# Performance work log

Hardware: AMD Instinct MI355X
Metric: run time of the kernel (lower is better)

Reference implementation:

```python
import jax, jax.numpy as jnp
import numpy as np

B, N, C = 16, 1024, 256
E = 524288
NUM_NODES = B * N
D0 = C + 7            # 263 input node feature dim
LAYERS = [256, 256, 256]


def _xavier(key, shape):
    fan_out, fan_in = shape
    lim = jnp.sqrt(6.0 / (fan_in + fan_out))
    return jax.random.uniform(key, shape, jnp.float32, -lim, lim)


def setup_inputs() -> dict:
    key = jax.random.key(0)
    ks = jax.random.split(key, 9)
    rois = jax.random.normal(ks[0], (B, N, 7), jnp.float32)
    pooled_features = jax.random.normal(ks[1], (B, N, C), jnp.float32)
    edge_index = jax.random.randint(ks[2], (2, E), 0, NUM_NODES, dtype=jnp.int64)
    # EdgeConv linear weights: layer0 in = 2*(C+7)=526, later in = 2*256=512
    W1 = _xavier(ks[3], (LAYERS[0], 2 * D0))
    b1 = jnp.zeros((LAYERS[0],), jnp.float32)
    W2 = _xavier(ks[4], (LAYERS[1], 2 * LAYERS[0]))
    b2 = jnp.zeros((LAYERS[1],), jnp.float32)
    W3 = _xavier(ks[5], (LAYERS[2], 2 * LAYERS[1]))
    b3 = jnp.zeros((LAYERS[2],), jnp.float32)
    return {"rois": rois, "pooled_features": pooled_features,
            "edge_index": edge_index,
            "W1": W1, "b1": b1, "W2": W2, "b2": b2, "W3": W3, "b3": b3}


def _edge_conv(x, src, dst, W, b):
    # message: cat(x_j - x_i, x_i) -> linear -> relu ; aggregate: scatter max at target i
    x_i = x[dst]                                   # [E, d] target features
    x_j = x[src]                                   # [E, d] source features
    msg = jnp.concatenate([x_j - x_i, x_i], axis=-1)   # [E, 2d]
    msg = jax.nn.relu(msg @ W.T + b)               # [E, out]
    agg = jax.ops.segment_max(msg, dst, num_segments=NUM_NODES)
    # nodes with no incoming edges: fill -inf -> 0 (PyG convention)
    return jnp.where(jnp.isfinite(agg), agg, jnp.zeros((), agg.dtype))


def reference(rois, pooled_features, edge_index, W1, b1, W2, b2, W3, b3):
    # global features: cat(pooled, boxes) flattened over batch
    x = jnp.concatenate([pooled_features, rois], axis=-1).reshape(-1, D0)  # [B*N, 263]
    src, dst = edge_index[0], edge_index[1]  # PyG: row = source j, col = target i
    feats = [x]
    x1 = _edge_conv(x, src, dst, W1, b1)
    feats.append(x1)
    x2 = _edge_conv(x1, src, dst, W2, b2)
    feats.append(x2)
    x3 = _edge_conv(x2, src, dst, W3, b3)
    feats.append(x3)
    related_features = jnp.concatenate(feats, axis=-1)  # [B*N, 263+768]
    return related_features
```

## Files before the change

kernel.cpp:

```cpp
#include <hip/hip_runtime.h>
#include <stdint.h>

#define NODES 16384
#define D0    263
#define K1PAD 288
#define OUTW  1031

typedef __attribute__((ext_vector_type(8))) short bf16x8;
typedef __attribute__((ext_vector_type(4))) float f32x4;

__device__ __forceinline__ float bf2f(unsigned short u) {
    union { unsigned int i; float f; } c; c.i = ((unsigned int)u) << 16; return c.f;
}
__device__ __forceinline__ unsigned short f2bf(float f) {
    union { float f; unsigned int i; } c; c.f = f;
    unsigned int x = c.i;
    unsigned int r = (x + 0x7fffu + ((x >> 16) & 1u)) >> 16;
    return (unsigned short)r;
}

__global__ void detect_kernel(const void* __restrict__ ei, const void* __restrict__ pooled,
                              int* __restrict__ flags) {
    int lane = threadIdx.x;
    const long long* e64 = (const long long*)ei;
    bool ok = true;
    for (int i = lane; i < 512; i += 64) {
        long long v = e64[i];
        if (v < 0 || v >= NODES) ok = false;
    }
    unsigned long long b = __ballot(ok);
    const unsigned short* ph = (const unsigned short*)pooled;
    int hits = 0;
    for (int i = lane; i < 512; i += 64) {
        int e = (ph[i] >> 7) & 0xFF;
        if (e >= 0x90) hits++;
    }
    for (int off = 32; off; off >>= 1) hits += __shfl_down(hits, off);
    if (lane == 0) {
        flags[0] = (b == ~0ull) ? 1 : 0;
        flags[1] = (hits > 8) ? 1 : 0;
    }
}

__global__ void hist_kernel(const void* __restrict__ ei, int E, const int* __restrict__ flags,
                            int* __restrict__ deg) {
    int e = blockIdx.x * blockDim.x + threadIdx.x;
    if (e >= E) return;
    int d = flags[0] ? (int)((const long long*)ei)[(size_t)E + e]
                     : ((const int*)ei)[(size_t)E + e];
    atomicAdd(&deg[d], 1);
}

__global__ void scan_kernel(const int* __restrict__ deg, int* __restrict__ offs,
                            int* __restrict__ cursor) {
    __shared__ int part[256];
    int tid = threadIdx.x;
    int base = tid * 64;
    int s = 0;
    for (int i = 0; i < 64; ++i) s += deg[base + i];
    part[tid] = s;
    __syncthreads();
    for (int off = 1; off < 256; off <<= 1) {
        int t = (tid >= off) ? part[tid - off] : 0;
        __syncthreads();
        part[tid] += t;
        __syncthreads();
    }
    int run = (tid > 0) ? part[tid - 1] : 0;
    for (int i = 0; i < 64; ++i) {
        int idx = base + i;
        offs[idx] = run;
        cursor[idx] = run;
        run += deg[idx];
    }
    if (tid == 255) offs[NODES] = run;
}

__global__ void scatter_kernel(const void* __restrict__ ei, int E, const int* __restrict__ flags,
                               int* __restrict__ cursor, int* __restrict__ ssrc) {
    int e = blockIdx.x * blockDim.x + threadIdx.x;
    if (e >= E) return;
    int s, d;
    if (flags[0]) {
        const long long* p = (const long long*)ei;
        s = (int)p[e];
        d = (int)p[(size_t)E + e];
    } else {
        const int* p = (const int*)ei;
        s = p[e];
        d = p[(size_t)E + e];
    }
    int pos = atomicAdd(&cursor[d], 1);
    ssrc[pos] = s;
}

__global__ void build_x0_kernel(const void* __restrict__ pooled, const void* __restrict__ rois,
                                const int* __restrict__ flags,
                                unsigned short* __restrict__ x0p, void* __restrict__ outv) {
    int idx = blockIdx.x * blockDim.x + threadIdx.x;
    int node = idx / K1PAD;
    int k = idx - node * K1PAD;
    if (node >= NODES) return;
    bool f32m = flags[1] != 0;
    float val = 0.f;
    if (k < 256) {
        val = f32m ? ((const float*)pooled)[(size_t)node * 256 + k]
                   : bf2f(((const unsigned short*)pooled)[(size_t)node * 256 + k]);
    } else if (k < D0) {
        val = f32m ? ((const float*)rois)[(size_t)node * 7 + (k - 256)]
                   : bf2f(((const unsigned short*)rois)[(size_t)node * 7 + (k - 256)]);
    }
    x0p[idx] = f2bf(val);
    if (k < D0) {
        if (f32m) ((float*)outv)[(size_t)node * OUTW + k] = val;
        else      ((unsigned short*)outv)[(size_t)node * OUTW + k] = f2bf(val);
    }
}

#define S1 (512 * K1PAD)
#define S2 (512 * 256)
__global__ void prep_all_kernel(const void* __restrict__ W1, const void* __restrict__ W2,
                                const void* __restrict__ W3, const int* __restrict__ flags,
                                unsigned short* __restrict__ wc1,
                                unsigned short* __restrict__ wc2,
                                unsigned short* __restrict__ wc3) {
    int idx = blockIdx.x * blockDim.x + threadIdx.x;
    bool f32m = flags[1] != 0;
    if (idx < S1) {
        int r = idx / K1PAD;
        int k = idx - r * K1PAD;
        unsigned short val = 0;
        if (k < D0) {
            if (r < 256) {
                float a = f32m ? ((const float*)W1)[(size_t)r * 526 + k]
                               : bf2f(((const unsigned short*)W1)[(size_t)r * 526 + k]);
                val = f2bf(a);
            } else {
                size_t ro = (size_t)(r - 256) * 526;
                float a, b;
                if (f32m) { a = ((const float*)W1)[ro + k]; b = ((const float*)W1)[ro + D0 + k]; }
                else      { a = bf2f(((const unsigned short*)W1)[ro + k]);
                            b = bf2f(((const unsigned short*)W1)[ro + D0 + k]); }
                val = f2bf(b - a);
            }
        }
        wc1[idx] = val;
        return;
    }
    idx -= S1;
    const void* W = (idx < S2) ? W2 : W3;
    unsigned short* wc = (idx < S2) ? wc2 : wc3;
    if (idx >= S2) idx -= S2;
    if (idx >= S2) return;
    int r = idx >> 8;
    int k = idx & 255;
    unsigned short val;
    if (r < 256) {
        float a = f32m ? ((const float*)W)[(size_t)r * 512 + k]
                       : bf2f(((const unsigned short*)W)[(size_t)r * 512 + k]);
        val = f2bf(a);
    } else {
        size_t ro = (size_t)(r - 256) * 512;
        float a, b;
        if (f32m) { a = ((const float*)W)[ro + k]; b = ((const float*)W)[ro + 256 + k]; }
        else      { a = bf2f(((const unsigned short*)W)[ro + k]);
                    b = bf2f(((const unsigned short*)W)[ro + 256 + k]); }
        val = f2bf(b - a);
    }
    wc[idx] = val;
}

template <int K>
__global__ __launch_bounds__(256) void gemm_kernel(const unsigned short* __restrict__ A,
                                                   const unsigned short* __restrict__ Wc,
                                                   unsigned short* __restrict__ u_bf,
                                                   float* __restrict__ v_f) {
    int lane = threadIdx.x & 63;
    int wave = threadIdx.x >> 6;
    int row0 = blockIdx.x * 64;
    int col0 = blockIdx.y * 256 + wave * 64;
    int lr = lane & 15;
    int kb = (lane >> 4) * 8;
    const unsigned short* Ap = A + (size_t)(row0 + lr) * K + kb;
    const unsigned short* Wp = Wc + (size_t)(col0 + lr) * K + kb;

    f32x4 acc[4][4];
    #pragma unroll
    for (int i = 0; i < 4; ++i)
        #pragma unroll
        for (int j = 0; j < 4; ++j) acc[i][j] = (f32x4){0.f, 0.f, 0.f, 0.f};

    for (int k0 = 0; k0 < K; k0 += 32) {
        bf16x8 a[4], b[4];
        #pragma unroll
        for (int i = 0; i < 4; ++i) a[i] = *reinterpret_cast<const bf16x8*>(Ap + (size_t)i * 16 * K + k0);
        #pragma unroll
        for (int i = 0; i < 4; ++i) b[i] = *reinterpret_cast<const bf16x8*>(Wp + (size_t)i * 16 * K + k0);
        #pragma unroll
        for (int rb = 0; rb < 4; ++rb)
            #pragma unroll
            for (int cb = 0; cb < 4; ++cb)
                acc[rb][cb] = __builtin_amdgcn_mfma_f32_16x16x32_bf16(a[rb], b[cb], acc[rb][cb], 0, 0, 0);
    }

    bool is_u = (blockIdx.y == 0);
    #pragma unroll
    for (int rb = 0; rb < 4; ++rb) {
        int rbase = row0 + rb * 16 + (lane >> 4) * 4;
        #pragma unroll
        for (int cb = 0; cb < 4; ++cb) {
            int c = col0 + cb * 16 + lr;
            #pragma unroll
            for (int reg = 0; reg < 4; ++reg) {
                float val = acc[rb][cb][reg];
                int r = rbase + reg;
                if (is_u) u_bf[(size_t)r * 256 + c] = f2bf(val);
                else      v_f[(size_t)r * 256 + (c - 256)] = val;
            }
        }
    }
}

__device__ __forceinline__ void maxpack2(float m[8], uint4 p, uint4 q) {
    unsigned pp[4] = {p.x, p.y, p.z, p.w};
    unsigned qq[4] = {q.x, q.y, q.z, q.w};
    #pragma unroll
    for (int w = 0; w < 4; ++w) {
        m[2 * w]     = fmaxf(fmaxf(m[2 * w],     bf2f((unsigned short)(pp[w] & 0xffff))),
                             bf2f((unsigned short)(qq[w] & 0xffff)));
        m[2 * w + 1] = fmaxf(fmaxf(m[2 * w + 1], bf2f((unsigned short)(pp[w] >> 16))),
                             bf2f((unsigned short)(qq[w] >> 16)));
    }
}
__device__ __forceinline__ void maxpack1(float m[8], uint4 p) {
    unsigned pp[4] = {p.x, p.y, p.z, p.w};
    #pragma unroll
    for (int w = 0; w < 4; ++w) {
        m[2 * w]     = fmaxf(m[2 * w],     bf2f((unsigned short)(pp[w] & 0xffff)));
        m[2 * w + 1] = fmaxf(m[2 * w + 1], bf2f((unsigned short)(pp[w] >> 16)));
    }
}

__global__ __launch_bounds__(256) void combine_kernel(const unsigned short* __restrict__ u_bf,
                                                      const float* __restrict__ v_f,
                                                      const void* __restrict__ bias,
                                                      const int* __restrict__ flags,
                                                      const int* __restrict__ offs,
                                                      const int* __restrict__ ssrc,
                                                      unsigned short* __restrict__ x_cur,
                                                      void* __restrict__ outv,
                                                      int col_off) {
    int lane = threadIdx.x & 63;
    int node = blockIdx.x * 4 + (threadIdx.x >> 6);
    int half = lane >> 5;
    int cl = lane & 31;
    int s0 = offs[node];
    int s1 = offs[node + 1];
    bool f32m = flags[1] != 0;

    const uint4* U = (const uint4*)u_bf;
    float m[8];
    #pragma unroll
    for (int j = 0; j < 8; ++j) m[j] = -INFINITY;

    int i = s0 + half;
    for (; i + 6 < s1; i += 8) {
        int sA = ssrc[i], sB = ssrc[i + 2], sC = ssrc[i + 4], sD = ssrc[i + 6];
        uint4 pA = U[(size_t)sA * 32 + cl];
        uint4 pB = U[(size_t)sB * 32 + cl];
        uint4 pC = U[(size_t)sC * 32 + cl];
        uint4 pD = U[(size_t)sD * 32 + cl];
        maxpack2(m, pA, pB);
        maxpack2(m, pC, pD);
    }
    for (; i < s1; i += 2) {
        int s = ssrc[i];
        maxpack1(m, U[(size_t)s * 32 + cl]);
    }

    #pragma unroll
    for (int j = 0; j < 8; ++j) m[j] = fmaxf(m[j], __shfl_xor(m[j], 32));

    int ch0 = cl * 8 + half * 4;
    float mm[4] = {m[half * 4 + 0], m[half * 4 + 1], m[half * 4 + 2], m[half * 4 + 3]};
    float4 v = *(const float4*)(v_f + (size_t)node * 256 + ch0);
    float bb[4];
    if (f32m) {
        const float* bf = (const float*)bias;
        #pragma unroll
        for (int j = 0; j < 4; ++j) bb[j] = bf[ch0 + j];
    } else {
        const unsigned short* bh = (const unsigned short*)bias;
        #pragma unroll
        for (int j = 0; j < 4; ++j) bb[j] = bf2f(bh[ch0 + j]);
    }
    float vv[4] = {v.x, v.y, v.z, v.w};
    float r[4];
    bool nz = (s1 > s0);
    #pragma unroll
    for (int j = 0; j < 4; ++j) r[j] = nz ? fmaxf(mm[j] + vv[j] + bb[j], 0.f) : 0.f;

    unsigned short h[4];
    #pragma unroll
    for (int j = 0; j < 4; ++j) h[j] = f2bf(r[j]);
    uint2 packed;
    packed.x = (unsigned int)h[0] | ((unsigned int)h[1] << 16);
    packed.y = (unsigned int)h[2] | ((unsigned int)h[3] << 16);
    *(uint2*)(x_cur + (size_t)node * 256 + ch0) = packed;

    size_t ob = (size_t)node * OUTW + col_off + ch0;
    if (f32m) {
        float* of = (float*)outv;
        #pragma unroll
        for (int j = 0; j < 4; ++j) of[ob + j] = r[j];
    } else {
        unsigned short* oh = (unsigned short*)outv;
        #pragma unroll
        for (int j = 0; j < 4; ++j) oh[ob + j] = h[j];
    }
}

extern "C" void kernel_launch(void* const* d_in, const int* in_sizes, int n_in,
                              void* d_out, int out_size, void* d_ws, size_t ws_size,
                              hipStream_t stream) {
    const void* rois   = d_in[0];
    const void* pooled = d_in[1];
    const void* ei     = d_in[2];
    const void* W1 = d_in[3];
    const void* b1 = d_in[4];
    const void* W2 = d_in[5];
    const void* b2 = d_in[6];
    const void* W3 = d_in[7];
    const void* b3 = d_in[8];

    const int E = in_sizes[2] / 2;

    char* ws = (char*)d_ws;
    size_t o = 0;
    auto take = [&](size_t bytes) { size_t cur = o; o += (bytes + 255) & ~(size_t)255; return cur; };
    int* flags           = (int*)(ws + take(8));
    int* deg             = (int*)(ws + take(sizeof(int) * NODES));
    int* offs            = (int*)(ws + take(sizeof(int) * (NODES + 1)));
    int* cursor          = (int*)(ws + take(sizeof(int) * NODES));
    int* ssrc            = (int*)(ws + take(sizeof(int) * (size_t)E));
    unsigned short* x0p  = (unsigned short*)(ws + take(2ull * NODES * K1PAD));
    unsigned short* wc1  = (unsigned short*)(ws + take(2ull * 512 * K1PAD));
    unsigned short* wc2  = (unsigned short*)(ws + take(2ull * 512 * 256));
    unsigned short* wc3  = (unsigned short*)(ws + take(2ull * 512 * 256));
    unsigned short* ubf  = (unsigned short*)(ws + take(2ull * NODES * 256));
    float*          vf   = (float*)(ws + take(4ull * NODES * 256));
    unsigned short* xcur = (unsigned short*)(ws + take(2ull * NODES * 256));
    (void)ws_size;

    const int eb = (E + 255) / 256;

    detect_kernel<<<1, 64, 0, stream>>>(ei, pooled, flags);
    hipMemsetAsync(deg, 0, sizeof(int) * NODES, stream);
    hist_kernel<<<eb, 256, 0, stream>>>(ei, E, flags, deg);
    scan_kernel<<<1, 256, 0, stream>>>(deg, offs, cursor);
    scatter_kernel<<<eb, 256, 0, stream>>>(ei, E, flags, cursor, ssrc);

    build_x0_kernel<<<(NODES * K1PAD) / 256, 256, 0, stream>>>(pooled, rois, flags, x0p, d_out);
    prep_all_kernel<<<(S1 + 2 * S2 + 255) / 256, 256, 0, stream>>>(W1, W2, W3, flags, wc1, wc2, wc3);

    gemm_kernel<K1PAD><<<dim3(NODES / 64, 2), 256, 0, stream>>>(x0p, wc1, ubf, vf);
    combine_kernel<<<NODES / 4, 256, 0, stream>>>(ubf, vf, b1, flags, offs, ssrc, xcur, d_out, D0);

    gemm_kernel<256><<<dim3(NODES / 64, 2), 256, 0, stream>>>(xcur, wc2, ubf, vf);
    combine_kernel<<<NODES / 4, 256, 0, stream>>>(ubf, vf, b2, flags, offs, ssrc, xcur, d_out, D0 + 256);

    gemm_kernel<256><<<dim3(NODES / 64, 2), 256, 0, stream>>>(xcur, wc3, ubf, vf);
    combine_kernel<<<NODES / 4, 256, 0, stream>>>(ubf, vf, b3, flags, offs, ssrc, xcur, d_out, D0 + 512);
}
```

Baseline: 258.3 us.

## Store GEMM u-output as order-preserving uint16 keys and fuse setup launches

```diff
diff --git a/kernel.cpp b/kernel.cpp
--- a/kernel.cpp
+++ b/kernel.cpp
@@ -8,6 +8,7 @@
 
 typedef __attribute__((ext_vector_type(8))) short bf16x8;
 typedef __attribute__((ext_vector_type(4))) float f32x4;
+typedef __attribute__((ext_vector_type(8))) unsigned short u16x8;
 
 __device__ __forceinline__ float bf2f(unsigned short u) {
     union { unsigned int i; float f; } c; c.i = ((unsigned int)u) << 16; return c.f;
@@ -18,27 +19,37 @@
     unsigned int r = (x + 0x7fffu + ((x >> 16) & 1u)) >> 16;
     return (unsigned short)r;
 }
-
-__global__ void detect_kernel(const void* __restrict__ ei, const void* __restrict__ pooled,
-                              int* __restrict__ flags) {
-    int lane = threadIdx.x;
-    const long long* e64 = (const long long*)ei;
-    bool ok = true;
-    for (int i = lane; i < 512; i += 64) {
-        long long v = e64[i];
-        if (v < 0 || v >= NODES) ok = false;
-    }
-    unsigned long long b = __ballot(ok);
-    const unsigned short* ph = (const unsigned short*)pooled;
-    int hits = 0;
-    for (int i = lane; i < 512; i += 64) {
-        int e = (ph[i] >> 7) & 0xFF;
-        if (e >= 0x90) hits++;
-    }
-    for (int off = 32; off; off >>= 1) hits += __shfl_down(hits, off);
-    if (lane == 0) {
-        flags[0] = (b == ~0ull) ? 1 : 0;
-        flags[1] = (hits > 8) ? 1 : 0;
+__device__ __forceinline__ unsigned short bf2key(unsigned short b) {
+    return (b & 0x8000u) ? (unsigned short)~b : (unsigned short)(b | 0x8000u);
+}
+__device__ __forceinline__ unsigned short key2bf(unsigned short k) {
+    return (k & 0x8000u) ? (unsigned short)(k ^ 0x8000u) : (unsigned short)~k;
+}
+
+__global__ void detect_zero_kernel(const void* __restrict__ ei, const void* __restrict__ pooled,
+                                   int* __restrict__ flags, int* __restrict__ deg) {
+    int idx = blockIdx.x * 256 + threadIdx.x;
+    deg[idx] = 0;
+    if (blockIdx.x == 0 && threadIdx.x < 64) {
+        int lane = threadIdx.x;
+        const long long* e64 = (const long long*)ei;
+        bool ok = true;
+        for (int i = lane; i < 512; i += 64) {
+            long long v = e64[i];
+            if (v < 0 || v >= NODES) ok = false;
+        }
+        unsigned long long b = __ballot(ok);
+        const unsigned short* ph = (const unsigned short*)pooled;
+        int hits = 0;
+        for (int i = lane; i < 512; i += 64) {
+            int e = (ph[i] >> 7) & 0xFF;
+            if (e >= 0x90) hits++;
+        }
+        for (int off = 32; off; off >>= 1) hits += __shfl_down(hits, off);
+        if (lane == 0) {
+            flags[0] = (b == ~0ull) ? 1 : 0;
+            flags[1] = (hits > 8) ? 1 : 0;
+        }
     }
 }
 
@@ -94,38 +105,36 @@
     ssrc[pos] = s;
 }
 
-__global__ void build_x0_kernel(const void* __restrict__ pooled, const void* __restrict__ rois,
-                                const int* __restrict__ flags,
-                                unsigned short* __restrict__ x0p, void* __restrict__ outv) {
-    int idx = blockIdx.x * blockDim.x + threadIdx.x;
-    int node = idx / K1PAD;
-    int k = idx - node * K1PAD;
-    if (node >= NODES) return;
-    bool f32m = flags[1] != 0;
-    float val = 0.f;
-    if (k < 256) {
-        val = f32m ? ((const float*)pooled)[(size_t)node * 256 + k]
-                   : bf2f(((const unsigned short*)pooled)[(size_t)node * 256 + k]);
-    } else if (k < D0) {
-        val = f32m ? ((const float*)rois)[(size_t)node * 7 + (k - 256)]
-                   : bf2f(((const unsigned short*)rois)[(size_t)node * 7 + (k - 256)]);
-    }
-    x0p[idx] = f2bf(val);
-    if (k < D0) {
-        if (f32m) ((float*)outv)[(size_t)node * OUTW + k] = val;
-        else      ((unsigned short*)outv)[(size_t)node * OUTW + k] = f2bf(val);
-    }
-}
-
+#define T0 (NODES * K1PAD)
 #define S1 (512 * K1PAD)
 #define S2 (512 * 256)
-__global__ void prep_all_kernel(const void* __restrict__ W1, const void* __restrict__ W2,
-                                const void* __restrict__ W3, const int* __restrict__ flags,
-                                unsigned short* __restrict__ wc1,
-                                unsigned short* __restrict__ wc2,
-                                unsigned short* __restrict__ wc3) {
-    int idx = blockIdx.x * blockDim.x + threadIdx.x;
+__global__ void setup_kernel(const void* __restrict__ pooled, const void* __restrict__ rois,
+                             const void* __restrict__ W1, const void* __restrict__ W2,
+                             const void* __restrict__ W3, const int* __restrict__ flags,
+                             unsigned short* __restrict__ x0p, void* __restrict__ outv,
+                             unsigned short* __restrict__ wc1, unsigned short* __restrict__ wc2,
+                             unsigned short* __restrict__ wc3) {
+    int idx = blockIdx.x * 256 + threadIdx.x;
     bool f32m = flags[1] != 0;
+    if (idx < T0) {
+        int node = idx / K1PAD;
+        int k = idx - node * K1PAD;
+        float val = 0.f;
+        if (k < 256) {
+            val = f32m ? ((const float*)pooled)[(size_t)node * 256 + k]
+                       : bf2f(((const unsigned short*)pooled)[(size_t)node * 256 + k]);
+        } else if (k < D0) {
+            val = f32m ? ((const float*)rois)[(size_t)node * 7 + (k - 256)]
+                       : bf2f(((const unsigned short*)rois)[(size_t)node * 7 + (k - 256)]);
+        }
+        x0p[idx] = f2bf(val);
+        if (k < D0) {
+            if (f32m) ((float*)outv)[(size_t)node * OUTW + k] = val;
+            else      ((unsigned short*)outv)[(size_t)node * OUTW + k] = f2bf(val);
+        }
+        return;
+    }
+    idx -= T0;
     if (idx < S1) {
         int r = idx / K1PAD;
         int k = idx - r * K1PAD;
@@ -151,7 +160,6 @@
     const void* W = (idx < S2) ? W2 : W3;
     unsigned short* wc = (idx < S2) ? wc2 : wc3;
     if (idx >= S2) idx -= S2;
-    if (idx >= S2) return;
     int r = idx >> 8;
     int k = idx & 255;
     unsigned short val;
@@ -173,7 +181,7 @@
 template <int K>
 __global__ __launch_bounds__(256) void gemm_kernel(const unsigned short* __restrict__ A,
                                                    const unsigned short* __restrict__ Wc,
-                                                   unsigned short* __restrict__ u_bf,
+                                                   unsigned short* __restrict__ u_key,
                                                    float* __restrict__ v_f) {
     int lane = threadIdx.x & 63;
     int wave = threadIdx.x >> 6;
@@ -214,34 +222,14 @@
             for (int reg = 0; reg < 4; ++reg) {
                 float val = acc[rb][cb][reg];
                 int r = rbase + reg;
-                if (is_u) u_bf[(size_t)r * 256 + c] = f2bf(val);
+                if (is_u) u_key[(size_t)r * 256 + c] = bf2key(f2bf(val));
                 else      v_f[(size_t)r * 256 + (c - 256)] = val;
             }
         }
     }
 }
 
-__device__ __forceinline__ void maxpack2(float m[8], uint4 p, uint4 q) {
-    unsigned pp[4] = {p.x, p.y, p.z, p.w};
-    unsigned qq[4] = {q.x, q.y, q.z, q.w};
-    #pragma unroll
-    for (int w = 0; w < 4; ++w) {
-        m[2 * w]     = fmaxf(fmaxf(m[2 * w],     bf2f((unsigned short)(pp[w] & 0xffff))),
-                             bf2f((unsigned short)(qq[w] & 0xffff)));
-        m[2 * w + 1] = fmaxf(fmaxf(m[2 * w + 1], bf2f((unsigned short)(pp[w] >> 16))),
-                             bf2f((unsigned short)(qq[w] >> 16)));
-    }
-}
-__device__ __forceinline__ void maxpack1(float m[8], uint4 p) {
-    unsigned pp[4] = {p.x, p.y, p.z, p.w};
-    #pragma unroll
-    for (int w = 0; w < 4; ++w) {
-        m[2 * w]     = fmaxf(m[2 * w],     bf2f((unsigned short)(pp[w] & 0xffff)));
-        m[2 * w + 1] = fmaxf(m[2 * w + 1], bf2f((unsigned short)(pp[w] >> 16)));
-    }
-}
-
-__global__ __launch_bounds__(256) void combine_kernel(const unsigned short* __restrict__ u_bf,
+__global__ __launch_bounds__(256) void combine_kernel(const unsigned short* __restrict__ u_key,
                                                       const float* __restrict__ v_f,
                                                       const void* __restrict__ bias,
                                                       const int* __restrict__ flags,
@@ -258,31 +246,37 @@
     int s1 = offs[node + 1];
     bool f32m = flags[1] != 0;
 
-    const uint4* U = (const uint4*)u_bf;
-    float m[8];
-    #pragma unroll
-    for (int j = 0; j < 8; ++j) m[j] = -INFINITY;
+    const u16x8* U = (const u16x8*)u_key;
+    u16x8 mk = (u16x8)0;
 
     int i = s0 + half;
     for (; i + 6 < s1; i += 8) {
         int sA = ssrc[i], sB = ssrc[i + 2], sC = ssrc[i + 4], sD = ssrc[i + 6];
-        uint4 pA = U[(size_t)sA * 32 + cl];
-        uint4 pB = U[(size_t)sB * 32 + cl];
-        uint4 pC = U[(size_t)sC * 32 + cl];
-        uint4 pD = U[(size_t)sD * 32 + cl];
-        maxpack2(m, pA, pB);
-        maxpack2(m, pC, pD);
+        u16x8 pA = U[(size_t)sA * 32 + cl];
+        u16x8 pB = U[(size_t)sB * 32 + cl];
+        u16x8 pC = U[(size_t)sC * 32 + cl];
+        u16x8 pD = U[(size_t)sD * 32 + cl];
+        mk = __builtin_elementwise_max(mk, __builtin_elementwise_max(
+                 __builtin_elementwise_max(pA, pB), __builtin_elementwise_max(pC, pD)));
     }
     for (; i < s1; i += 2) {
         int s = ssrc[i];
-        maxpack1(m, U[(size_t)s * 32 + cl]);
-    }
-
-    #pragma unroll
-    for (int j = 0; j < 8; ++j) m[j] = fmaxf(m[j], __shfl_xor(m[j], 32));
+        mk = __builtin_elementwise_max(mk, U[(size_t)s * 32 + cl]);
+    }
+
+    union { u16x8 v; uint4 u; } cvt;
+    cvt.v = mk;
+    cvt.u.x = __shfl_xor((int)cvt.u.x, 32);
+    cvt.u.y = __shfl_xor((int)cvt.u.y, 32);
+    cvt.u.z = __shfl_xor((int)cvt.u.z, 32);
+    cvt.u.w = __shfl_xor((int)cvt.u.w, 32);
+    mk = __builtin_elementwise_max(mk, cvt.v);
 
     int ch0 = cl * 8 + half * 4;
-    float mm[4] = {m[half * 4 + 0], m[half * 4 + 1], m[half * 4 + 2], m[half * 4 + 3]};
+    float mm[4];
+    #pragma unroll
+    for (int j = 0; j < 4; ++j) mm[j] = bf2f(key2bf(mk[half * 4 + j]));
+
     float4 v = *(const float4*)(v_f + (size_t)node * 256 + ch0);
     float bb[4];
     if (f32m) {
@@ -347,28 +341,27 @@
     unsigned short* wc1  = (unsigned short*)(ws + take(2ull * 512 * K1PAD));
     unsigned short* wc2  = (unsigned short*)(ws + take(2ull * 512 * 256));
     unsigned short* wc3  = (unsigned short*)(ws + take(2ull * 512 * 256));
-    unsigned short* ubf  = (unsigned short*)(ws + take(2ull * NODES * 256));
+    unsigned short* ukey = (unsigned short*)(ws + take(2ull * NODES * 256));
     float*          vf   = (float*)(ws + take(4ull * NODES * 256));
     unsigned short* xcur = (unsigned short*)(ws + take(2ull * NODES * 256));
     (void)ws_size;
 
     const int eb = (E + 255) / 256;
 
-    detect_kernel<<<1, 64, 0, stream>>>(ei, pooled, flags);
-    hipMemsetAsync(deg, 0, sizeof(int) * NODES, stream);
+    detect_zero_kernel<<<NODES / 256, 256, 0, stream>>>(ei, pooled, flags, deg);
     hist_kernel<<<eb, 256, 0, stream>>>(ei, E, flags, deg);
     scan_kernel<<<1, 256, 0, stream>>>(deg, offs, cursor);
     scatter_kernel<<<eb, 256, 0, stream>>>(ei, E, flags, cursor, ssrc);
 
-    build_x0_kernel<<<(NODES * K1PAD) / 256, 256, 0, stream>>>(pooled, rois, flags, x0p, d_out);
-    prep_all_kernel<<<(S1 + 2 * S2 + 255) / 256, 256, 0, stream>>>(W1, W2, W3, flags, wc1, wc2, wc3);
-
-    gemm_kernel<K1PAD><<<dim3(NODES / 64, 2), 256, 0, stream>>>(x0p, wc1, ubf, vf);
-    combine_kernel<<<NODES / 4, 256, 0, stream>>>(ubf, vf, b1, flags, offs, ssrc, xcur, d_out, D0);
-
-    gemm_kernel<256><<<dim3(NODES / 64, 2), 256, 0, stream>>>(xcur, wc2, ubf, vf);
-    combine_kernel<<<NODES / 4, 256, 0, stream>>>(ubf, vf, b2, flags, offs, ssrc, xcur, d_out, D0 + 256);
-
-    gemm_kernel<256><<<dim3(NODES / 64, 2), 256, 0, stream>>>(xcur, wc3, ubf, vf);
-    combine_kernel<<<NODES / 4, 256, 0, stream>>>(ubf, vf, b3, flags, offs, ssrc, xcur, d_out, D0 + 512);
-}
+    setup_kernel<<<(T0 + S1 + 2 * S2) / 256, 256, 0, stream>>>(pooled, rois, W1, W2, W3, flags,
+                                                               x0p, d_out, wc1, wc2, wc3);
+
+    gemm_kernel<K1PAD><<<dim3(NODES / 64, 2), 256, 0, stream>>>(x0p, wc1, ukey, vf);
+    combine_kernel<<<NODES / 4, 256, 0, stream>>>(ukey, vf, b1, flags, offs, ssrc, xcur, d_out, D0);
+
+    gemm_kernel<256><<<dim3(NODES / 64, 2), 256, 0, stream>>>(xcur, wc2, ukey, vf);
+    combine_kernel<<<NODES / 4, 256, 0, stream>>>(ukey, vf, b2, flags, offs, ssrc, xcur, d_out, D0 + 256);
+
+    gemm_kernel<256><<<dim3(NODES / 64, 2), 256, 0, stream>>>(xcur, wc3, ukey, vf);
+    combine_kernel<<<NODES / 4, 256, 0, stream>>>(ukey, vf, b3, flags, offs, ssrc, xcur, d_out, D0 + 512);
+}
```

Measured after the change: 252.7 us. 1.02x faster.
